# Optimization experiments

Hardware: AMD Instinct MI355X
Metric: run time of the kernel (lower is better)

Reference implementation:

```python
import jax, jax.numpy as jnp
import numpy as np

B, N, INDIM = 512, 200, 200
D1, D2, D3 = 32, 32, 8
RATIO = 0.5
K1 = int(np.ceil(RATIO * N))    # 100 nodes kept after pool1
K2 = int(np.ceil(RATIO * K1))   # 50 nodes kept after pool2
BN_EPS = 1e-5
NEG = -1e9


def setup_inputs() -> dict:
    key = jax.random.key(0)
    ks = jax.random.split(key, 16)
    x = jax.random.normal(ks[0], (B, N, INDIM), jnp.float32)
    u = jax.random.uniform(ks[1], (B, N, N), jnp.float32)
    ut = jnp.triu(jnp.where(u > 0.9, u, 0.0), 1)
    adj = ut + jnp.swapaxes(ut, 1, 2)
    g = lambda i, shape: jax.random.normal(ks[i], shape, jnp.float32) * 0.1
    return dict(
        x=x, adj=adj,
        W1=g(2, (INDIM, D1)), a1s=g(3, (D1,)), a1d=g(4, (D1,)), b1=jnp.zeros((D1,), jnp.float32),
        W2=g(5, (D1, D2)), a2s=g(6, (D2,)), a2d=g(7, (D2,)), b2=jnp.zeros((D2,), jnp.float32),
        pw1=g(8, (D1,)), pw2=g(9, (D2,)),
        fc1_w=g(10, ((D1 + D2) * 2, D2)), fc1_b=jnp.zeros((D2,), jnp.float32),
        fc2_w=g(11, (D2, D3)), fc2_b=jnp.zeros((D3,), jnp.float32),
        fc3_w=g(12, (D3, 2)), fc3_b=jnp.zeros((2,), jnp.float32),
        bn4_g=jnp.ones((D2,), jnp.float32), bn4_b=jnp.zeros((D2,), jnp.float32),
        bn5_g=jnp.ones((D3,), jnp.float32), bn5_b=jnp.zeros((D3,), jnp.float32))


def _gat(x, mask, W, a_s, a_d, b):
    # PyG GATConv (heads=1): alpha_ij = softmax_j LeakyReLU(a_d.h_i + a_s.h_j) over in-neighbors j (self-loops added)
    h = jnp.einsum('bnf,fd->bnd', x, W)
    es = h @ a_s                    # [B,n] source term
    ed = h @ a_d                    # [B,n] dest term
    m = mask | jnp.eye(mask.shape[1], dtype=bool)
    logits = jax.nn.leaky_relu(ed[:, :, None] + es[:, None, :], 0.2)
    alpha = jax.nn.softmax(jnp.where(m, logits, NEG), axis=-1)   # [B,n,n]
    return jnp.einsum('bij,bjd->bid', alpha, h) + b


def _topk(x, adj_w, w, k):
    # TopKPooling(multiplier=1, nonlinearity=sigmoid): score = sigmoid(x.w/||w||)
    score = jax.nn.sigmoid((x @ w) / (jnp.linalg.norm(w) + 1e-16))   # [B,n]
    vals, idx = jax.lax.top_k(score, k)                              # perm sorted desc, as PyG
    xk = jnp.take_along_axis(x, idx[:, :, None], axis=1) * vals[:, :, None]
    ak = jnp.take_along_axis(jnp.take_along_axis(adj_w, idx[:, :, None], axis=1), idx[:, None, :], axis=2)
    return xk, ak, vals


def _bn(z, g, b):
    # eval-mode BatchNorm1d: running_mean=0, running_var=1
    return g * z / jnp.sqrt(1.0 + BN_EPS) + b


def reference(x, adj, W1, a1s, a1d, b1, W2, a2s, a2d, b2, pw1, pw2,
              fc1_w, fc1_b, fc2_w, fc2_b, fc3_w, fc3_b, bn4_g, bn4_b, bn5_g, bn5_b):
    h = _gat(x, adj > 0, W1, a1s, a1d, b1)
    h, aw, s1 = _topk(h, adj, pw1, K1)
    x1 = jnp.concatenate([h.max(axis=1), h.mean(axis=1)], axis=1)    # [B, 64]
    # augment_adj: add self-loops, spspmm (A+I)@(A+I), remove self-loops
    eye = jnp.eye(K1, dtype=aw.dtype)
    a2 = jnp.einsum('bij,bjk->bik', aw + eye, aw + eye) * (1.0 - eye)
    h = _gat(h, a2 != 0, W2, a2s, a2d, b2)
    h, _, s2 = _topk(h, a2, pw2, K2)
    x2 = jnp.concatenate([h.max(axis=1), h.mean(axis=1)], axis=1)    # [B, 64]
    z = jnp.concatenate([x1, x2], axis=1)                            # [B, 128]
    z = _bn(jax.nn.relu(z @ fc1_w + fc1_b), bn4_g, bn4_b)            # dropout: eval -> identity
    z = _bn(jax.nn.relu(z @ fc2_w + fc2_b), bn5_g, bn5_b)
    logp = jax.nn.log_softmax(z @ fc3_w + fc3_b, axis=-1)            # [B, 2]
    return logp, s1, s2
```

## Files before the change

kernel.cpp:

```cpp
#include <hip/hip_runtime.h>
#include <math.h>

#define N_   200
#define B_   512
#define K1_  100
#define K2_  50

#define S1_OFF 1024
#define S2_OFF 52224

__device__ __forceinline__ float lrelu(float v) { return v > 0.f ? v : 0.2f * v; }
__device__ __forceinline__ float sigm(float v)  { return 1.f / (1.f + __expf(-v)); }

__device__ __forceinline__ void bitonic_desc(float* key, int* idx, int n, int t) {
  for (int k = 2; k <= n; k <<= 1) {
    for (int j = k >> 1; j > 0; j >>= 1) {
      __syncthreads();
      int ixj = t ^ j;
      if (t < n && ixj > t) {
        float a = key[t], c = key[ixj];
        int ia = idx[t], ic = idx[ixj];
        bool gt = (a > c) || (a == c && ia < ic);
        if (((t & k) == 0) ? !gt : gt) {
          key[t] = c; key[ixj] = a; idx[t] = ic; idx[ixj] = ia;
        }
      }
    }
  }
  __syncthreads();
}


__global__ __launch_bounds__(256) void gnn_fused(
    const float* __restrict__ x, const float* __restrict__ adj,
    const float* __restrict__ W1, const float* __restrict__ a1s,
    const float* __restrict__ a1d, const float* __restrict__ b1,
    const float* __restrict__ W2g, const float* __restrict__ a2s,
    const float* __restrict__ a2d, const float* __restrict__ b2,
    const float* __restrict__ pw1, const float* __restrict__ pw2,
    const float* __restrict__ fc1w, const float* __restrict__ fc1b,
    const float* __restrict__ fc2w, const float* __restrict__ fc2b,
    const float* __restrict__ fc3w, const float* __restrict__ fc3b,
    const float* __restrict__ bn4g, const float* __restrict__ bn4b,
    const float* __restrict__ bn5g, const float* __restrict__ bn5b,
    float* __restrict__ out)
{
  __shared__ __align__(16) char smem[63792];
  float*    sH    = (float*)smem;
  float*    sH1   = (float*)(smem + 25600);
  float*    sXK   = (float*)(smem + 38400);
  float*    sES   = (float*)(smem + 51200);
  float*    sED   = (float*)(smem + 52000);
  unsigned* sBITS = (unsigned*)(smem + 52800);
  float*    sW2   = (float*)(smem + 52800);
  float*    sKey  = (float*)(smem + 58400);
  int*      sIdx  = (int*)(smem + 59424);
  int*      sSel  = (int*)(smem + 60448);
  float*    sVal  = (float*)(smem + 60848);
  float*    sXV   = (float*)(smem + 61248);
  float*    sRed  = (float*)(smem + 61760);
  unsigned* sMask2= (unsigned*)(smem + 61792);

  const int t = threadIdx.x;
  const int b = blockIdx.x;
  const float* xb = x   + (size_t)b * N_ * N_;
  const float* ab = adj + (size_t)b * N_ * N_;

  if (t < N_) {
    float acc[32];
    #pragma unroll
    for (int d = 0; d < 32; ++d) acc[d] = 0.f;
    const float* xr = xb + t * N_;
    for (int k = 0; k < N_; k += 4) {
      float4 xv = *(const float4*)(xr + k);
      #pragma unroll
      for (int kk = 0; kk < 4; ++kk) {
        float xs = (&xv.x)[kk];
        const float* wr = W1 + (k + kk) * 32;
        #pragma unroll
        for (int d = 0; d < 32; ++d) acc[d] += xs * wr[d];
      }
    }
    float es = 0.f, ed = 0.f;
    #pragma unroll
    for (int d = 0; d < 32; ++d) { es += acc[d] * a1s[d]; ed += acc[d] * a1d[d]; }
    sES[t] = es; sED[t] = ed;
    #pragma unroll
    for (int d = 0; d < 32; ++d) sH[t * 32 + d] = acc[d];
  }
  __syncthreads();

  {
    float v = (t < N_) ? sES[t] : -3.0e38f;
    #pragma unroll
    for (int off = 1; off < 64; off <<= 1) v = fmaxf(v, __shfl_xor(v, off, 64));
    if ((t & 63) == 0) sRed[t >> 6] = v;
  }
  __syncthreads();
  {
    float esmax = fmaxf(fmaxf(sRed[0], sRed[1]), fmaxf(sRed[2], sRed[3]));

    if (t < N_) {
      const float* arow = ab + (size_t)t * N_;
      float ed_i = sED[t];
      float L = lrelu(ed_i + esmax);
      float ssum = 0.f;
      float acc[32];
      #pragma unroll
      for (int d = 0; d < 32; ++d) acc[d] = 0.f;
      for (int jw = 0; jw < 7; ++jw) {
        int jbase = jw * 32;
        int cnt = (jw < 6) ? 32 : 8;
        unsigned mb = 0u;
        for (int j4 = 0; j4 < cnt; j4 += 4) {
          float4 av = *(const float4*)(arow + jbase + j4);
          #pragma unroll
          for (int jj = 0; jj < 4; ++jj) {
            int j = jbase + j4 + jj;
            float a = (&av.x)[jj];
            bool conn = a > 0.f;
            if (conn) mb |= (1u << (j4 + jj));
            float w = 0.f;
            if (conn || j == t) w = __expf(lrelu(ed_i + sES[j]) - L);
            ssum += w;
            const float* hr = &sH[j * 32];
            #pragma unroll
            for (int d = 0; d < 32; ++d) acc[d] += w * hr[d];
          }
        }
        sBITS[t * 7 + jw] = mb;
      }
      float inv = 1.f / ssum;
      #pragma unroll
      for (int d = 0; d < 32; ++d) sH1[t * 32 + d] = acc[d] * inv + b1[d];
    }
  }
  __syncthreads();

  {
    float npw = 0.f;
    #pragma unroll
    for (int d = 0; d < 32; ++d) npw += pw1[d] * pw1[d];
    npw = sqrtf(npw) + 1e-16f;
    float sc = -1.f;
    if (t < N_) {
      float dp = 0.f;
      #pragma unroll
      for (int d = 0; d < 32; ++d) dp += sH1[t * 32 + d] * pw1[d];
      sc = sigm(dp / npw);
    }
    sKey[t] = sc; sIdx[t] = t;
  }
  bitonic_desc(sKey, sIdx, 256, t);
  if (t < K1_) {
    out[S1_OFF + b * K1_ + t] = sKey[t];
    sVal[t] = sKey[t]; sSel[t] = sIdx[t];
  }
  __syncthreads();
  {
    float tmp[13];
    #pragma unroll
    for (int it = 0; it < 13; ++it) {
      int i = t + it * 256;
      if (i < K1_ * 32) tmp[it] = sH1[sSel[i >> 5] * 32 + (i & 31)] * sVal[i >> 5];
    }
    __syncthreads();
    #pragma unroll
    for (int it = 0; it < 13; ++it) {
      int i = t + it * 256;
      if (i < K1_ * 32) sXK[i] = tmp[it];
    }
  }
  __syncthreads();
  if (t < 32) {
    float m = -3.0e38f, s = 0.f;
    for (int r = 0; r < K1_; ++r) { float v = sXK[r * 32 + t]; m = fmaxf(m, v); s += v; }
    sXV[t] = m; sXV[32 + t] = s / 100.f;
  }

  if (t < K1_) {
    int gi = sSel[t];
    #pragma unroll
    for (int w = 0; w < 4; ++w) {
      unsigned m = 0;
      const int lim = (w < 3) ? 32 : 4;
      for (int jj = 0; jj < lim; ++jj) {
        int j = w * 32 + jj;
        int gj = sSel[j];
        unsigned bit = (sBITS[gi * 7 + (gj >> 5)] >> (gj & 31)) & 1u;
        if (j == t) bit = 1u;
        m |= bit << jj;
      }
      sMask2[t * 5 + w] = m;
    }
  }
  __syncthreads();
  {
    unsigned pr0 = 0, pr1 = 0, pr2 = 0, pr3 = 0;
    if (t < K1_) {
      #pragma unroll
      for (int kw = 0; kw < 4; ++kw) {
        unsigned mk = sMask2[t * 5 + kw];
        const int lim = (kw < 3) ? 32 : 4;
        for (int kk = 0; kk < lim; ++kk) {
          if ((mk >> kk) & 1u) {
            int k = kw * 32 + kk;
            pr0 |= sMask2[k * 5 + 0]; pr1 |= sMask2[k * 5 + 1];
            pr2 |= sMask2[k * 5 + 2]; pr3 |= sMask2[k * 5 + 3];
          }
        }
      }
    }
    __syncthreads();
    if (t < K1_) {
      sMask2[t * 5 + 0] = pr0; sMask2[t * 5 + 1] = pr1;
      sMask2[t * 5 + 2] = pr2; sMask2[t * 5 + 3] = pr3;
    }
  }
  __syncthreads();

  for (int i = t; i < 1024; i += 256) sW2[i] = W2g[i];
  __syncthreads();
  if (t < K1_) {
    float acc[32];
    #pragma unroll
    for (int d = 0; d < 32; ++d) acc[d] = 0.f;
    for (int k = 0; k < 32; ++k) {
      float xv = sXK[t * 32 + k];
      const float* wr = &sW2[k * 32];
      #pragma unroll
      for (int d = 0; d < 32; ++d) acc[d] += xv * wr[d];
    }
    float es = 0.f, ed = 0.f;
    #pragma unroll
    for (int d = 0; d < 32; ++d) { es += acc[d] * a2s[d]; ed += acc[d] * a2d[d]; }
    sES[t] = es; sED[t] = ed;
    #pragma unroll
    for (int d = 0; d < 32; ++d) sH[t * 32 + d] = acc[d];
  }
  __syncthreads();
  {
    float v = (t < K1_) ? sES[t] : -3.0e38f;
    #pragma unroll
    for (int off = 1; off < 64; off <<= 1) v = fmaxf(v, __shfl_xor(v, off, 64));
    if ((t & 63) == 0) sRed[t >> 6] = v;
  }
  __syncthreads();
  {
    float esm2 = fmaxf(fmaxf(sRed[0], sRed[1]), fmaxf(sRed[2], sRed[3]));
    if (t < K1_) {
      float ed_i = sED[t];
      float L = lrelu(ed_i + esm2);
      float ssum = 0.f;
      float acc[32];
      #pragma unroll
      for (int d = 0; d < 32; ++d) acc[d] = 0.f;
      #pragma unroll
      for (int jw = 0; jw < 4; ++jw) {
        unsigned mw = sMask2[t * 5 + jw];
        const int lim = (jw < 3) ? 32 : 4;
        for (int jj = 0; jj < lim; ++jj) {
          int j = jw * 32 + jj;
          float w = 0.f;
          if ((mw >> jj) & 1u) w = __expf(lrelu(ed_i + sES[j]) - L);
          ssum += w;
          const float* hr = &sH[j * 32];
          #pragma unroll
          for (int d = 0; d < 32; ++d) acc[d] += w * hr[d];
        }
      }
      float inv = 1.f / ssum;
      #pragma unroll
      for (int d = 0; d < 32; ++d) sH1[t * 32 + d] = acc[d] * inv + b2[d];
    }
  }
  __syncthreads();

  {
    float npw = 0.f;
    #pragma unroll
    for (int d = 0; d < 32; ++d) npw += pw2[d] * pw2[d];
    npw = sqrtf(npw) + 1e-16f;
    float sc = -1.f;
    if (t < K1_) {
      float dp = 0.f;
      #pragma unroll
      for (int d = 0; d < 32; ++d) dp += sH1[t * 32 + d] * pw2[d];
      sc = sigm(dp / npw);
    }
    if (t < 128) { sKey[t] = sc; sIdx[t] = t; }
  }
  bitonic_desc(sKey, sIdx, 128, t);
  if (t < K2_) {
    out[S2_OFF + b * K2_ + t] = sKey[t];
    sVal[t] = sKey[t]; sSel[t] = sIdx[t];
  }
  __syncthreads();
  {
    int d = t & 31, r0 = t >> 5;
    for (int r = r0; r < K2_; r += 8) sXK[r * 32 + d] = sH1[sSel[r] * 32 + d] * sVal[r];
  }
  __syncthreads();
  if (t < 32) {
    float m = -3.0e38f, s = 0.f;
    for (int r = 0; r < K2_; ++r) { float v = sXK[r * 32 + t]; m = fmaxf(m, v); s += v; }
    sXV[64 + t] = m; sXV[96 + t] = s / 50.f;
  }
  __syncthreads();

  const float RS = 0.99999500003749969f;
  if (t < 32) {
    float z = fc1b[t];
    for (int k = 0; k < 128; ++k) z += sXV[k] * fc1w[k * 32 + t];
    z = fmaxf(z, 0.f);
    z = bn4g[t] * z * RS + bn4b[t];
    sKey[t] = z;
  }
  __syncthreads();
  if (t < 8) {
    float z = fc2b[t];
    for (int k = 0; k < 32; ++k) z += sKey[k] * fc2w[k * 8 + t];
    z = fmaxf(z, 0.f);
    z = bn5g[t] * z * RS + bn5b[t];
    sKey[32 + t] = z;
  }
  __syncthreads();
  if (t < 2) {
    float z = fc3b[t];
    for (int k = 0; k < 8; ++k) z += sKey[32 + k] * fc3w[k * 2 + t];
    sKey[40 + t] = z;
  }
  __syncthreads();
  if (t < 2) {
    float z0 = sKey[40], z1 = sKey[41];
    float m = fmaxf(z0, z1);
    float lse = m + logf(__expf(z0 - m) + __expf(z1 - m));
    out[b * 2 + t] = sKey[40 + t] - lse;
  }
}

extern "C" void kernel_launch(void* const* d_in, const int* in_sizes, int n_in,
                              void* d_out, int out_size, void* d_ws, size_t ws_size,
                              hipStream_t stream) {
  (void)in_sizes; (void)n_in; (void)d_ws; (void)ws_size; (void)out_size;
  const float* x    = (const float*)d_in[0];
  const float* adj  = (const float*)d_in[1];
  const float* W1   = (const float*)d_in[2];
  const float* a1s  = (const float*)d_in[3];
  const float* a1d  = (const float*)d_in[4];
  const float* b1   = (const float*)d_in[5];
  const float* W2   = (const float*)d_in[6];
  const float* a2s  = (const float*)d_in[7];
  const float* a2d  = (const float*)d_in[8];
  const float* b2   = (const float*)d_in[9];
  const float* pw1  = (const float*)d_in[10];
  const float* pw2  = (const float*)d_in[11];
  const float* fc1w = (const float*)d_in[12];
  const float* fc1b = (const float*)d_in[13];
  const float* fc2w = (const float*)d_in[14];
  const float* fc2b = (const float*)d_in[15];
  const float* fc3w = (const float*)d_in[16];
  const float* fc3b = (const float*)d_in[17];
  const float* bn4g = (const float*)d_in[18];
  const float* bn4b = (const float*)d_in[19];
  const float* bn5g = (const float*)d_in[20];
  const float* bn5b = (const float*)d_in[21];

  gnn_fused<<<B_, 256, 0, stream>>>(x, adj, W1, a1s, a1d, b1, W2, a2s, a2d, b2,
                                    pw1, pw2, fc1w, fc1b, fc2w, fc2b, fc3w, fc3b,
                                    bn4g, bn4b, bn5g, bn5b, (float*)d_out);
}
```

Before: 334.3 us.

## Stage x tiles in LDS for coalesced GAT1 projection and precompute adjacency bitmask

The first GAT projection now copies 32-row tiles of x into shared memory with coalesced float4 loads. Eight threads cooperate per row, each owning four output dims, and the attention dot products are reduced with shuffles. The adjacency bitmask is built up front by all 256 threads with coalesced reads, so the attention loop reads bits from LDS instead of strided global rows. This targets the uncoalesced per-thread row reads of x and adj, and in exchange adds extra block barriers and reuses the sH1 region as a staging buffer.

```diff
diff --git a/kernel.cpp b/kernel.cpp
--- a/kernel.cpp
+++ b/kernel.cpp
@@ -48,6 +48,7 @@
   __shared__ __align__(16) char smem[63792];
   float*    sH    = (float*)smem;
   float*    sH1   = (float*)(smem + 25600);
+  float*    sXt   = (float*)(smem + 25600);
   float*    sXK   = (float*)(smem + 38400);
   float*    sES   = (float*)(smem + 51200);
   float*    sED   = (float*)(smem + 52000);
@@ -66,27 +67,66 @@
   const float* xb = x   + (size_t)b * N_ * N_;
   const float* ab = adj + (size_t)b * N_ * N_;
 
-  if (t < N_) {
-    float acc[32];
-    #pragma unroll
-    for (int d = 0; d < 32; ++d) acc[d] = 0.f;
-    const float* xr = xb + t * N_;
-    for (int k = 0; k < N_; k += 4) {
-      float4 xv = *(const float4*)(xr + k);
-      #pragma unroll
-      for (int kk = 0; kk < 4; ++kk) {
-        float xs = (&xv.x)[kk];
-        const float* wr = W1 + (k + kk) * 32;
+  for (int wi = t; wi < 1400; wi += 256) {
+    int row = wi / 7;
+    int w   = wi - row * 7;
+    const float* p = ab + row * N_ + w * 32;
+    unsigned m = 0u;
+    if (w < 6) {
+      #pragma unroll
+      for (int e = 0; e < 32; e += 4) {
+        float4 v = *(const float4*)(p + e);
+        m |= (unsigned)(v.x > 0.f) << e;
+        m |= (unsigned)(v.y > 0.f) << (e + 1);
+        m |= (unsigned)(v.z > 0.f) << (e + 2);
+        m |= (unsigned)(v.w > 0.f) << (e + 3);
+      }
+    } else {
+      #pragma unroll
+      for (int e = 0; e < 8; e += 4) {
+        float4 v = *(const float4*)(p + e);
+        m |= (unsigned)(v.x > 0.f) << e;
+        m |= (unsigned)(v.y > 0.f) << (e + 1);
+        m |= (unsigned)(v.z > 0.f) << (e + 2);
+        m |= (unsigned)(v.w > 0.f) << (e + 3);
+      }
+    }
+    sBITS[row * 7 + w] = m;
+  }
+
+  {
+    const int r  = t >> 3;
+    const int d0 = (t & 7) * 4;
+    const float4 as4 = *(const float4*)(a1s + d0);
+    const float4 ad4 = *(const float4*)(a1d + d0);
+    for (int T = 0; T < 7; ++T) {
+      const int r0   = T * 32;
+      const int rows = (T < 6) ? 32 : 8;
+      __syncthreads();
+      const float4* src = (const float4*)(xb + r0 * N_);
+      for (int i = t; i < rows * 50; i += 256) ((float4*)sXt)[i] = src[i];
+      __syncthreads();
+      if (r < rows) {
+        float4 acc = make_float4(0.f, 0.f, 0.f, 0.f);
+        const float* xr = sXt + r * N_;
+        #pragma unroll 4
+        for (int k = 0; k < N_; ++k) {
+          float xv = xr[k];
+          float4 wv = *(const float4*)(W1 + k * 32 + d0);
+          acc.x += xv * wv.x; acc.y += xv * wv.y;
+          acc.z += xv * wv.z; acc.w += xv * wv.w;
+        }
+        *(float4*)(sH + (r0 + r) * 32 + d0) = acc;
+        float esP = acc.x * as4.x + acc.y * as4.y + acc.z * as4.z + acc.w * as4.w;
+        float edP = acc.x * ad4.x + acc.y * ad4.y + acc.z * ad4.z + acc.w * ad4.w;
         #pragma unroll
-        for (int d = 0; d < 32; ++d) acc[d] += xs * wr[d];
-      }
-    }
-    float es = 0.f, ed = 0.f;
-    #pragma unroll
-    for (int d = 0; d < 32; ++d) { es += acc[d] * a1s[d]; ed += acc[d] * a1d[d]; }
-    sES[t] = es; sED[t] = ed;
-    #pragma unroll
-    for (int d = 0; d < 32; ++d) sH[t * 32 + d] = acc[d];
+        for (int off = 1; off < 8; off <<= 1) {
+          esP += __shfl_xor(esP, off, 64);
+          edP += __shfl_xor(edP, off, 64);
+        }
+        if ((t & 7) == 0) { sES[r0 + r] = esP; sED[r0 + r] = edP; }
+      }
+    }
   }
   __syncthreads();
 
@@ -101,7 +141,6 @@
     float esmax = fmaxf(fmaxf(sRed[0], sRed[1]), fmaxf(sRed[2], sRed[3]));
 
     if (t < N_) {
-      const float* arow = ab + (size_t)t * N_;
       float ed_i = sED[t];
       float L = lrelu(ed_i + esmax);
       float ssum = 0.f;
@@ -109,26 +148,17 @@
       #pragma unroll
       for (int d = 0; d < 32; ++d) acc[d] = 0.f;
       for (int jw = 0; jw < 7; ++jw) {
-        int jbase = jw * 32;
-        int cnt = (jw < 6) ? 32 : 8;
-        unsigned mb = 0u;
-        for (int j4 = 0; j4 < cnt; j4 += 4) {
-          float4 av = *(const float4*)(arow + jbase + j4);
+        unsigned mb = sBITS[t * 7 + jw];
+        const int cnt = (jw < 6) ? 32 : 8;
+        for (int jj = 0; jj < cnt; ++jj) {
+          int j = jw * 32 + jj;
+          float w = 0.f;
+          if (((mb >> jj) & 1u) || j == t) w = __expf(lrelu(ed_i + sES[j]) - L);
+          ssum += w;
+          const float* hr = &sH[j * 32];
           #pragma unroll
-          for (int jj = 0; jj < 4; ++jj) {
-            int j = jbase + j4 + jj;
-            float a = (&av.x)[jj];
-            bool conn = a > 0.f;
-            if (conn) mb |= (1u << (j4 + jj));
-            float w = 0.f;
-            if (conn || j == t) w = __expf(lrelu(ed_i + sES[j]) - L);
-            ssum += w;
-            const float* hr = &sH[j * 32];
-            #pragma unroll
-            for (int d = 0; d < 32; ++d) acc[d] += w * hr[d];
-          }
-        }
-        sBITS[t * 7 + jw] = mb;
+          for (int d = 0; d < 32; ++d) acc[d] += w * hr[d];
+        }
       }
       float inv = 1.f / ssum;
       #pragma unroll
```

New measurement: 507.8 us. +51.9%, slower.

## Repartition GAT aggregation across all threads and precompute adjacency bitmasks

Applied to the files above, without the earlier changes.

Adjacency bitmasks are now built up front by all 256 threads with coalesced float4 reads, instead of per row inside the attention loop. Both GAT aggregation stages now split each row's 32 output features across 4 lane groups, with each thread covering several rows. This uses all four waves and vectorized shared-memory reads in place of 200 or 100 threads each holding a 32-wide accumulator. The 2-hop mask product becomes a branch-free loop over uint4 rows with stride 8, and the stage-2 mask rows are cached in registers. The cost is recomputing the exp per feature group and a slightly larger shared-memory footprint.

```diff
diff --git a/kernel.cpp b/kernel.cpp
--- a/kernel.cpp
+++ b/kernel.cpp
@@ -45,7 +45,7 @@
     const float* __restrict__ bn5g, const float* __restrict__ bn5b,
     float* __restrict__ out)
 {
-  __shared__ __align__(16) char smem[63792];
+  __shared__ __align__(16) char smem[64992];
   float*    sH    = (float*)smem;
   float*    sH1   = (float*)(smem + 25600);
   float*    sXK   = (float*)(smem + 38400);
@@ -66,6 +66,22 @@
   const float* xb = x   + (size_t)b * N_ * N_;
   const float* ab = adj + (size_t)b * N_ * N_;
 
+  for (int wi = t; wi < 1400; wi += 256) {
+    int row = wi / 7;
+    int w   = wi - row * 7;
+    const float* p = ab + row * N_ + w * 32;
+    unsigned m = 0u;
+    const int lim = (w < 6) ? 32 : 8;
+    for (int e = 0; e < lim; e += 4) {
+      float4 v = *(const float4*)(p + e);
+      m |= (unsigned)(v.x > 0.f) << e;
+      m |= (unsigned)(v.y > 0.f) << (e + 1);
+      m |= (unsigned)(v.z > 0.f) << (e + 2);
+      m |= (unsigned)(v.w > 0.f) << (e + 3);
+    }
+    sBITS[row * 7 + w] = m;
+  }
+
   if (t < N_) {
     float acc[32];
     #pragma unroll
@@ -98,41 +114,70 @@
   }
   __syncthreads();
   {
-    float esmax = fmaxf(fmaxf(sRed[0], sRed[1]), fmaxf(sRed[2], sRed[3]));
-
-    if (t < N_) {
-      const float* arow = ab + (size_t)t * N_;
-      float ed_i = sED[t];
-      float L = lrelu(ed_i + esmax);
-      float ssum = 0.f;
-      float acc[32];
-      #pragma unroll
-      for (int d = 0; d < 32; ++d) acc[d] = 0.f;
-      for (int jw = 0; jw < 7; ++jw) {
-        int jbase = jw * 32;
-        int cnt = (jw < 6) ? 32 : 8;
-        unsigned mb = 0u;
-        for (int j4 = 0; j4 < cnt; j4 += 4) {
-          float4 av = *(const float4*)(arow + jbase + j4);
+    const float esmax = fmaxf(fmaxf(sRed[0], sRed[1]), fmaxf(sRed[2], sRed[3]));
+
+    const int wv = t >> 6;
+    const int lane = t & 63;
+    const int dg = lane >> 4;
+    const int rg = lane & 15;
+    const int rbase = wv * 50;
+    int   rowc[4]; bool val[4];
+    float edv[4], Lv[4], ssum[4];
+    float acc[4][8];
+    #pragma unroll
+    for (int rr = 0; rr < 4; ++rr) {
+      int rl = rg + 16 * rr;
+      val[rr] = rl < 50;
+      rowc[rr] = val[rr] ? (rbase + rl) : 0;
+      edv[rr] = sED[rowc[rr]];
+      Lv[rr]  = lrelu(edv[rr] + esmax);
+      ssum[rr] = 0.f;
+      #pragma unroll
+      for (int d = 0; d < 8; ++d) acc[rr][d] = 0.f;
+    }
+    for (int jw = 0; jw < 7; ++jw) {
+      unsigned mw[4];
+      #pragma unroll
+      for (int rr = 0; rr < 4; ++rr) {
+        mw[rr] = val[rr] ? sBITS[rowc[rr] * 7 + jw] : 0u;
+        if (val[rr] && (rowc[rr] >> 5) == jw) mw[rr] |= 1u << (rowc[rr] & 31);
+      }
+      const int cnt = (jw < 6) ? 32 : 8;
+      for (int jj4 = 0; jj4 < cnt; jj4 += 4) {
+        float4 esv = *(const float4*)&sES[jw * 32 + jj4];
+        #pragma unroll
+        for (int u = 0; u < 4; ++u) {
+          int jj = jj4 + u;
+          int j = jw * 32 + jj;
+          float esj = (&esv.x)[u];
+          float4 h0 = *(const float4*)&sH[j * 32 + dg * 8];
+          float4 h1v = *(const float4*)&sH[j * 32 + dg * 8 + 4];
           #pragma unroll
-          for (int jj = 0; jj < 4; ++jj) {
-            int j = jbase + j4 + jj;
-            float a = (&av.x)[jj];
-            bool conn = a > 0.f;
-            if (conn) mb |= (1u << (j4 + jj));
-            float w = 0.f;
-            if (conn || j == t) w = __expf(lrelu(ed_i + sES[j]) - L);
-            ssum += w;
-            const float* hr = &sH[j * 32];
-            #pragma unroll
-            for (int d = 0; d < 32; ++d) acc[d] += w * hr[d];
+          for (int rr = 0; rr < 4; ++rr) {
+            float w = ((mw[rr] >> jj) & 1u) ? __expf(lrelu(edv[rr] + esj) - Lv[rr]) : 0.f;
+            ssum[rr] += w;
+            acc[rr][0] += w * h0.x; acc[rr][1] += w * h0.y;
+            acc[rr][2] += w * h0.z; acc[rr][3] += w * h0.w;
+            acc[rr][4] += w * h1v.x; acc[rr][5] += w * h1v.y;
+            acc[rr][6] += w * h1v.z; acc[rr][7] += w * h1v.w;
           }
         }
-        sBITS[t * 7 + jw] = mb;
-      }
-      float inv = 1.f / ssum;
-      #pragma unroll
-      for (int d = 0; d < 32; ++d) sH1[t * 32 + d] = acc[d] * inv + b1[d];
+      }
+    }
+    float4 b1a = *(const float4*)(b1 + dg * 8);
+    float4 b1b = *(const float4*)(b1 + dg * 8 + 4);
+    #pragma unroll
+    for (int rr = 0; rr < 4; ++rr) {
+      if (val[rr]) {
+        float inv = 1.f / ssum[rr];
+        float4 o0, o1;
+        o0.x = acc[rr][0] * inv + b1a.x; o0.y = acc[rr][1] * inv + b1a.y;
+        o0.z = acc[rr][2] * inv + b1a.z; o0.w = acc[rr][3] * inv + b1a.w;
+        o1.x = acc[rr][4] * inv + b1b.x; o1.y = acc[rr][5] * inv + b1b.y;
+        o1.z = acc[rr][6] * inv + b1b.z; o1.w = acc[rr][7] * inv + b1b.w;
+        *(float4*)&sH1[rowc[rr] * 32 + dg * 8]     = o0;
+        *(float4*)&sH1[rowc[rr] * 32 + dg * 8 + 4] = o1;
+      }
     }
   }
   __syncthreads();
@@ -180,6 +225,9 @@
 
   if (t < K1_) {
     int gi = sSel[t];
+    unsigned bt[7];
+    #pragma unroll
+    for (int w = 0; w < 7; ++w) bt[w] = sBITS[gi * 7 + w];
     #pragma unroll
     for (int w = 0; w < 4; ++w) {
       unsigned m = 0;
@@ -187,34 +235,32 @@
       for (int jj = 0; jj < lim; ++jj) {
         int j = w * 32 + jj;
         int gj = sSel[j];
-        unsigned bit = (sBITS[gi * 7 + (gj >> 5)] >> (gj & 31)) & 1u;
+        unsigned bit = (bt[gj >> 5] >> (gj & 31)) & 1u;
         if (j == t) bit = 1u;
         m |= bit << jj;
       }
-      sMask2[t * 5 + w] = m;
+      sMask2[t * 8 + w] = m;
     }
   }
   __syncthreads();
   {
     unsigned pr0 = 0, pr1 = 0, pr2 = 0, pr3 = 0;
+    unsigned ow0 = 0, ow1 = 0, ow2 = 0, ow3 = 0;
     if (t < K1_) {
-      #pragma unroll
-      for (int kw = 0; kw < 4; ++kw) {
-        unsigned mk = sMask2[t * 5 + kw];
-        const int lim = (kw < 3) ? 32 : 4;
-        for (int kk = 0; kk < lim; ++kk) {
-          if ((mk >> kk) & 1u) {
-            int k = kw * 32 + kk;
-            pr0 |= sMask2[k * 5 + 0]; pr1 |= sMask2[k * 5 + 1];
-            pr2 |= sMask2[k * 5 + 2]; pr3 |= sMask2[k * 5 + 3];
-          }
-        }
-      }
+      ow0 = sMask2[t * 8 + 0]; ow1 = sMask2[t * 8 + 1];
+      ow2 = sMask2[t * 8 + 2]; ow3 = sMask2[t * 8 + 3];
+    }
+    for (int k = 0; k < K1_; ++k) {
+      uint4 mk = *(const uint4*)&sMask2[k * 8];
+      unsigned bit = (k < 32) ? (ow0 >> k) : (k < 64) ? (ow1 >> (k - 32))
+                   : (k < 96) ? (ow2 >> (k - 64)) : (ow3 >> (k - 96));
+      unsigned sel = (bit & 1u) ? 0xFFFFFFFFu : 0u;
+      pr0 |= mk.x & sel; pr1 |= mk.y & sel; pr2 |= mk.z & sel; pr3 |= mk.w & sel;
     }
     __syncthreads();
     if (t < K1_) {
-      sMask2[t * 5 + 0] = pr0; sMask2[t * 5 + 1] = pr1;
-      sMask2[t * 5 + 2] = pr2; sMask2[t * 5 + 3] = pr3;
+      sMask2[t * 8 + 0] = pr0; sMask2[t * 8 + 1] = pr1;
+      sMask2[t * 8 + 2] = pr2; sMask2[t * 8 + 3] = pr3;
     }
   }
   __syncthreads();
@@ -247,31 +293,67 @@
   }
   __syncthreads();
   {
-    float esm2 = fmaxf(fmaxf(sRed[0], sRed[1]), fmaxf(sRed[2], sRed[3]));
-    if (t < K1_) {
-      float ed_i = sED[t];
-      float L = lrelu(ed_i + esm2);
-      float ssum = 0.f;
-      float acc[32];
-      #pragma unroll
-      for (int d = 0; d < 32; ++d) acc[d] = 0.f;
-      #pragma unroll
-      for (int jw = 0; jw < 4; ++jw) {
-        unsigned mw = sMask2[t * 5 + jw];
-        const int lim = (jw < 3) ? 32 : 4;
-        for (int jj = 0; jj < lim; ++jj) {
+    const float esm2 = fmaxf(fmaxf(sRed[0], sRed[1]), fmaxf(sRed[2], sRed[3]));
+    const int wv = t >> 6;
+    const int lane = t & 63;
+    const int dg = lane >> 4;
+    const int rg = lane & 15;
+    const int rbase = wv * 25;
+    int   rowc[2]; bool val[2];
+    float edv[2], Lv[2], ssum[2];
+    float acc[2][8];
+    #pragma unroll
+    for (int rr = 0; rr < 2; ++rr) {
+      int rl = rg + 16 * rr;
+      val[rr] = rl < 25;
+      rowc[rr] = val[rr] ? (rbase + rl) : 0;
+      edv[rr] = sED[rowc[rr]];
+      Lv[rr]  = lrelu(edv[rr] + esm2);
+      ssum[rr] = 0.f;
+      #pragma unroll
+      for (int d = 0; d < 8; ++d) acc[rr][d] = 0.f;
+    }
+    for (int jw = 0; jw < 4; ++jw) {
+      unsigned mw[2];
+      #pragma unroll
+      for (int rr = 0; rr < 2; ++rr)
+        mw[rr] = val[rr] ? sMask2[rowc[rr] * 8 + jw] : 0u;
+      const int cnt = (jw < 3) ? 32 : 4;
+      for (int jj4 = 0; jj4 < cnt; jj4 += 4) {
+        float4 esv = *(const float4*)&sES[jw * 32 + jj4];
+        #pragma unroll
+        for (int u = 0; u < 4; ++u) {
+          int jj = jj4 + u;
           int j = jw * 32 + jj;
-          float w = 0.f;
-          if ((mw >> jj) & 1u) w = __expf(lrelu(ed_i + sES[j]) - L);
-          ssum += w;
-          const float* hr = &sH[j * 32];
+          float esj = (&esv.x)[u];
+          float4 h0 = *(const float4*)&sH[j * 32 + dg * 8];
+          float4 h1v = *(const float4*)&sH[j * 32 + dg * 8 + 4];
           #pragma unroll
-          for (int d = 0; d < 32; ++d) acc[d] += w * hr[d];
+          for (int rr = 0; rr < 2; ++rr) {
+            float w = ((mw[rr] >> jj) & 1u) ? __expf(lrelu(edv[rr] + esj) - Lv[rr]) : 0.f;
+            ssum[rr] += w;
+            acc[rr][0] += w * h0.x; acc[rr][1] += w * h0.y;
+            acc[rr][2] += w * h0.z; acc[rr][3] += w * h0.w;
+            acc[rr][4] += w * h1v.x; acc[rr][5] += w * h1v.y;
+            acc[rr][6] += w * h1v.z; acc[rr][7] += w * h1v.w;
+          }
         }
       }
-      float inv = 1.f / ssum;
-      #pragma unroll
-      for (int d = 0; d < 32; ++d) sH1[t * 32 + d] = acc[d] * inv + b2[d];
+    }
+    float4 b2a = *(const float4*)(b2 + dg * 8);
+    float4 b2b = *(const float4*)(b2 + dg * 8 + 4);
+    #pragma unroll
+    for (int rr = 0; rr < 2; ++rr) {
+      if (val[rr]) {
+        float inv = 1.f / ssum[rr];
+        float4 o0, o1;
+        o0.x = acc[rr][0] * inv + b2a.x; o0.y = acc[rr][1] * inv + b2a.y;
+        o0.z = acc[rr][2] * inv + b2a.z; o0.w = acc[rr][3] * inv + b2a.w;
+        o1.x = acc[rr][4] * inv + b2b.x; o1.y = acc[rr][5] * inv + b2b.y;
+        o1.z = acc[rr][6] * inv + b2b.z; o1.w = acc[rr][7] * inv + b2b.w;
+        *(float4*)&sH1[rowc[rr] * 32 + dg * 8]     = o0;
+        *(float4*)&sH1[rowc[rr] * 32 + dg * 8 + 4] = o1;
+      }
     }
   }
   __syncthreads();
```

Result: slower. 345.4 us (+3.3%).
